# Optimization experiments

Measured on AMD Instinct MI355X. Metric: run time of the kernel, lower is better.

Reference implementation:

```python
import jax, jax.numpy as jnp
import numpy as np

B, T, E = 8, 2048, 512   # batch, tokens, embedding_dim
K, C = 8192, 8           # num_embeddings, codebook_dim
LN_EPS = 1e-5


def _layer_norm(x, g, b):
    mu = jnp.mean(x, axis=-1, keepdims=True)
    var = jnp.var(x, axis=-1, keepdims=True)
    return (x - mu) * jax.lax.rsqrt(var + LN_EPS) * g + b


def setup_inputs() -> dict:
    key = jax.random.key(0)
    ks = jax.random.split(key, 8)
    s_e = 1.0 / np.sqrt(E)
    s_c = 1.0 / np.sqrt(C)
    return {
        "features": jax.random.normal(ks[0], (B, T, E), dtype=jnp.float32),
        # project_in: Linear(E,E) -> ReLU -> Linear(E,C)
        "W1_in": jax.random.uniform(ks[1], (E, E), jnp.float32, -s_e, s_e),
        "b1_in": jnp.zeros((E,), jnp.float32),
        "W2_in": jax.random.uniform(ks[2], (E, C), jnp.float32, -s_e, s_e),
        "b2_in": jnp.zeros((C,), jnp.float32),
        "ln_in_g": jnp.ones((C,), jnp.float32),
        "ln_in_b": jnp.zeros((C,), jnp.float32),
        # codebook
        "emb": jax.random.normal(ks[3], (K, C), dtype=jnp.float32),
        # project_out: Linear(C,E) -> ReLU -> Linear(E,E)
        "W1_out": jax.random.uniform(ks[4], (C, E), jnp.float32, -s_c, s_c),
        "b1_out": jnp.zeros((E,), jnp.float32),
        "W2_out": jax.random.uniform(ks[5], (E, E), jnp.float32, -s_e, s_e),
        "b2_out": jnp.zeros((E,), jnp.float32),
        "ln_out_g": jnp.ones((E,), jnp.float32),
        "ln_out_b": jnp.zeros((E,), jnp.float32),
    }


def reference(features, W1_in, b1_in, W2_in, b2_in, ln_in_g, ln_in_b, emb,
              W1_out, b1_out, W2_out, b2_out, ln_out_g, ln_out_b):
    # project_in + norm_in
    h = jax.nn.relu(jnp.einsum('bte,ef->btf', features, W1_in) + b1_in)
    z = jnp.einsum('bte,ec->btc', h, W2_in) + b2_in          # (B,T,C)
    z = _layer_norm(z, ln_in_g, ln_in_b)
    zf = z.reshape(-1, C)                                     # (N,C)
    d = (jnp.sum(zf * zf, axis=1, keepdims=True)
         - 2.0 * zf @ emb.T
         + jnp.sum(emb * emb, axis=1)[None, :])               # (N,K)
    idx = jnp.argmin(d, axis=1)                               # (N,)
    encodings = jax.nn.one_hot(idx, K, dtype=zf.dtype)        # (N,K)
    quantized = emb[idx]                                      # gather == one_hot @ emb
    # project_out + norm_out
    q = jax.nn.relu(quantized @ W1_out + b1_out)
    q = q @ W2_out + b2_out
    q = _layer_norm(q, ln_out_g, ln_out_b)
    q = q.reshape(B, T, E)
    return q, idx[:, None], encodings
```

## Files before the change

kernel.cpp:

```cpp
#include <hip/hip_runtime.h>
#include <cstdint>
#include <cstddef>

#define N_TOK 16384
#define E_DIM 512
#define C_DIM 8
#define K_CODES 8192
#define LN_EPS 1e-5f

typedef __attribute__((ext_vector_type(8))) short short8;
typedef __attribute__((ext_vector_type(4))) float f32x4;

__device__ __forceinline__ unsigned short bf16_rn(float x) {
  unsigned u = __float_as_uint(x);
  unsigned r = u + 0x7FFFu + ((u >> 16) & 1u);
  return (unsigned short)(r >> 16);
}
__device__ __forceinline__ float bf16_f(unsigned short h) {
  return __uint_as_float(((unsigned)h) << 16);
}

__device__ __forceinline__ void gload16(const void* g, void* l) {
  __builtin_amdgcn_global_load_lds(
      (const __attribute__((address_space(1))) void*)g,
      (__attribute__((address_space(3))) void*)l, 16, 0, 0);
}

__device__ __forceinline__ void pack_a_body(const float* __restrict__ A,
    unsigned short* __restrict__ hi, unsigned short* __restrict__ lo, int t) {
  int l = t & 63;
  int kt = (t >> 6) & 15;
  int mf = t >> 10;
  const float* src = A + (size_t)(mf * 16 + (l & 15)) * 512 + kt * 32 + (l >> 4) * 8;
  float4 x0 = *(const float4*)src;
  float4 x1 = *(const float4*)(src + 4);
  float xs[8] = {x0.x, x0.y, x0.z, x0.w, x1.x, x1.y, x1.z, x1.w};
  unsigned hw[4], lw[4];
#pragma unroll
  for (int p = 0; p < 4; ++p) {
    float a = xs[2 * p], b = xs[2 * p + 1];
    unsigned short ha = bf16_rn(a), hb = bf16_rn(b);
    unsigned short la = bf16_rn(a - bf16_f(ha)), lb = bf16_rn(b - bf16_f(hb));
    hw[p] = (unsigned)ha | ((unsigned)hb << 16);
    lw[p] = (unsigned)la | ((unsigned)lb << 16);
  }
  uint4 hv; hv.x = hw[0]; hv.y = hw[1]; hv.z = hw[2]; hv.w = hw[3];
  uint4 lv; lv.x = lw[0]; lv.y = lw[1]; lv.z = lw[2]; lv.w = lw[3];
  ((uint4*)hi)[t] = hv;
  ((uint4*)lo)[t] = lv;
}

__device__ __forceinline__ void pack_b_body(const float* __restrict__ B,
    unsigned short* __restrict__ hi, unsigned short* __restrict__ lo, int t) {
  int l = t & 63;
  int kt = (t >> 6) & 15;
  int nf = t >> 10;
  int col = nf * 16 + (l & 15);
  int krow = kt * 32 + (l >> 4) * 8;
  unsigned hw[4], lw[4];
#pragma unroll
  for (int p = 0; p < 4; ++p) {
    float a = B[(size_t)(krow + 2 * p) * 512 + col];
    float b = B[(size_t)(krow + 2 * p + 1) * 512 + col];
    unsigned short ha = bf16_rn(a), hb = bf16_rn(b);
    unsigned short la = bf16_rn(a - bf16_f(ha)), lb = bf16_rn(b - bf16_f(hb));
    hw[p] = (unsigned)ha | ((unsigned)hb << 16);
    lw[p] = (unsigned)la | ((unsigned)lb << 16);
  }
  uint4 hv; hv.x = hw[0]; hv.y = hw[1]; hv.z = hw[2]; hv.w = hw[3];
  uint4 lv; lv.x = lw[0]; lv.y = lw[1]; lv.z = lw[2]; lv.w = lw[3];
  ((uint4*)hi)[t] = hv;
  ((uint4*)lo)[t] = lv;
}

__global__ __launch_bounds__(256) void prep(const float* __restrict__ features,
    const float* __restrict__ W1_in, const float* __restrict__ W2_out,
    const float* __restrict__ emb,
    unsigned short* __restrict__ A1h, unsigned short* __restrict__ A1l,
    unsigned short* __restrict__ B1h, unsigned short* __restrict__ B1l,
    unsigned short* __restrict__ B2h, unsigned short* __restrict__ B2l,
    float* __restrict__ ne) {
  int bid = blockIdx.x;
  int tid = threadIdx.x;
  if (bid < 4096) {
    pack_a_body(features, A1h, A1l, bid * 256 + tid);
  } else if (bid < 4224) {
    pack_b_body(W1_in, B1h, B1l, (bid - 4096) * 256 + tid);
  } else if (bid < 4352) {
    pack_b_body(W2_out, B2h, B2l, (bid - 4224) * 256 + tid);
  } else {
    int k = (bid - 4352) * 256 + tid;
    const float* e = emb + (size_t)k * C_DIM;
    float s = 0.f;
#pragma unroll
    for (int c = 0; c < C_DIM; ++c) s = fmaf(e[c], e[c], s);
    ne[k] = s;
  }
}

template<bool RELU>
__global__ __launch_bounds__(256) void gemm_mfma(const unsigned short* __restrict__ Ah,
    const unsigned short* __restrict__ Al, const unsigned short* __restrict__ Bh,
    const unsigned short* __restrict__ Bl, const float* __restrict__ bias,
    float* __restrict__ C) {
  __shared__ char smem[65536];
  const int tid = threadIdx.x;
  const int l = tid & 63;
  const int w = tid >> 6;
  const int wm = w >> 1, wn = w & 1;
  const int mblk = blockIdx.y, nblk = blockIdx.x;

  const char* gAh = (const char*)Ah + (((size_t)(mblk * 8 + 2 * w) * 16) * 64 + l) * 16;
  const char* gAl = (const char*)Al + (((size_t)(mblk * 8 + 2 * w) * 16) * 64 + l) * 16;
  const char* gBh = (const char*)Bh + (((size_t)(nblk * 8 + 2 * w) * 16) * 64 + l) * 16;
  const char* gBl = (const char*)Bl + (((size_t)(nblk * 8 + 2 * w) * 16) * 64 + l) * 16;

  f32x4 acc[4][4];
#pragma unroll
  for (int i = 0; i < 4; ++i)
#pragma unroll
    for (int j = 0; j < 4; ++j) acc[i][j] = (f32x4){0.f, 0.f, 0.f, 0.f};

  auto stage = [&](int buf, int kt) {
    char* base = smem + buf * 32768;
    const size_t ko = (size_t)kt * 1024;
    char* dA0 = base + (2 * w) * 1024;
    char* dA1 = base + 8192 + (2 * w) * 1024;
    char* dB0 = base + 16384 + (2 * w) * 1024;
    char* dB1 = base + 24576 + (2 * w) * 1024;
    gload16(gAh + ko,         dA0);
    gload16(gAh + ko + 16384, dA0 + 1024);
    gload16(gAl + ko,         dA1);
    gload16(gAl + ko + 16384, dA1 + 1024);
    gload16(gBh + ko,         dB0);
    gload16(gBh + ko + 16384, dB0 + 1024);
    gload16(gBl + ko,         dB1);
    gload16(gBl + ko + 16384, dB1 + 1024);
  };

  auto compute = [&](int buf) {
    const char* base = smem + buf * 32768;
    const short8* sAh = (const short8*)(base);
    const short8* sAl = (const short8*)(base + 8192);
    const short8* sBh = (const short8*)(base + 16384);
    const short8* sBl = (const short8*)(base + 24576);
    short8 a_h[4], a_l[4], b_h[4], b_l[4];
#pragma unroll
    for (int i = 0; i < 4; ++i) {
      a_h[i] = sAh[(wm * 4 + i) * 64 + l];
      a_l[i] = sAl[(wm * 4 + i) * 64 + l];
    }
#pragma unroll
    for (int j = 0; j < 4; ++j) {
      b_h[j] = sBh[(wn * 4 + j) * 64 + l];
      b_l[j] = sBl[(wn * 4 + j) * 64 + l];
    }
#pragma unroll
    for (int i = 0; i < 4; ++i)
#pragma unroll
      for (int j = 0; j < 4; ++j) {
        acc[i][j] = __builtin_amdgcn_mfma_f32_16x16x32_bf16(a_h[i], b_h[j], acc[i][j], 0, 0, 0);
        acc[i][j] = __builtin_amdgcn_mfma_f32_16x16x32_bf16(a_h[i], b_l[j], acc[i][j], 0, 0, 0);
        acc[i][j] = __builtin_amdgcn_mfma_f32_16x16x32_bf16(a_l[i], b_h[j], acc[i][j], 0, 0, 0);
      }
  };

  stage(0, 0);
  __syncthreads();
  int cur = 0;
#pragma unroll 1
  for (int kt = 1; kt < 16; ++kt) {
    stage(cur ^ 1, kt);
    compute(cur);
    __syncthreads();
    cur ^= 1;
  }
  compute(cur);

  const int colb = nblk * 128 + wn * 64 + (l & 15);
  const int rowb = mblk * 128 + wm * 64 + ((l >> 4) << 2);
#pragma unroll
  for (int j = 0; j < 4; ++j) {
    float bv = bias[colb + j * 16];
#pragma unroll
    for (int i = 0; i < 4; ++i) {
#pragma unroll
      for (int r = 0; r < 4; ++r) {
        float v = acc[i][j][r] + bv;
        if (RELU) v = fmaxf(v, 0.f);
        C[(size_t)(rowb + i * 16 + r) * 512 + colb + j * 16] = v;
      }
    }
  }
}

__global__ __launch_bounds__(256) void zln_kernel(const float* __restrict__ h,
    const float* __restrict__ W2, const float* __restrict__ b2,
    const float* __restrict__ g, const float* __restrict__ b,
    float* __restrict__ z) {
  int token = blockIdx.x * 4 + (threadIdx.x >> 6);
  int lane = threadIdx.x & 63;
  const float* hr = h + (size_t)token * E_DIM;
  float acc[C_DIM];
#pragma unroll
  for (int c = 0; c < C_DIM; ++c) acc[c] = 0.f;
  for (int e = lane; e < E_DIM; e += 64) {
    float hv = hr[e];
    const float* w = W2 + e * C_DIM;
#pragma unroll
    for (int c = 0; c < C_DIM; ++c) acc[c] = fmaf(hv, w[c], acc[c]);
  }
#pragma unroll
  for (int c = 0; c < C_DIM; ++c) {
#pragma unroll
    for (int off = 32; off > 0; off >>= 1) acc[c] += __shfl_down(acc[c], off);
  }
  if (lane == 0) {
    float v[C_DIM]; float mu = 0.f;
#pragma unroll
    for (int c = 0; c < C_DIM; ++c) { v[c] = acc[c] + b2[c]; mu += v[c]; }
    mu *= 0.125f;
    float var = 0.f;
#pragma unroll
    for (int c = 0; c < C_DIM; ++c) { float d = v[c] - mu; var += d * d; }
    var *= 0.125f;
    float inv = 1.0f / sqrtf(var + LN_EPS);
#pragma unroll
    for (int c = 0; c < C_DIM; ++c)
      z[(size_t)token * C_DIM + c] = ((v[c] - mu) * inv) * g[c] + b[c];
  }
}

__global__ __launch_bounds__(256) void vq_partial(const float* __restrict__ z,
    const float* __restrict__ emb, const float* __restrict__ ne,
    float* __restrict__ pbest, int* __restrict__ pidx) {
  int chunk = blockIdx.x & 7;
  int token = (blockIdx.x >> 3) * 256 + threadIdx.x;
  float zv[C_DIM];
#pragma unroll
  for (int c = 0; c < C_DIM; ++c) zv[c] = z[(size_t)token * C_DIM + c];
  float s = 0.f;
#pragma unroll
  for (int c = 0; c < C_DIM; ++c) s = fmaf(zv[c], zv[c], s);
  float best = 3.402823466e38f; int bi = 0;
  int j0 = chunk * 1024;
  for (int j = j0; j < j0 + 1024; ++j) {
    const float* e = emb + (size_t)j * C_DIM;
    float p = 0.f;
#pragma unroll
    for (int c = 0; c < C_DIM; ++c) p = fmaf(zv[c], e[c], p);
    float d = fmaf(-2.f, p, s) + ne[j];
    if (d < best) { best = d; bi = j; }
  }
  pbest[chunk * N_TOK + token] = best;
  pidx[chunk * N_TOK + token] = bi;
}

__global__ void vq_combine(const float* __restrict__ pbest, const int* __restrict__ pidx,
    int* __restrict__ idx_i, float* __restrict__ idxf) {
  int n = blockIdx.x * 256 + threadIdx.x;
  float best = pbest[n]; int bi = pidx[n];
#pragma unroll
  for (int c = 1; c < 8; ++c) {
    float bb = pbest[c * N_TOK + n]; int i2 = pidx[c * N_TOK + n];
    if (bb < best) { best = bb; bi = i2; }
  }
  idx_i[n] = bi;
  idxf[n] = (float)bi;
}

__global__ __launch_bounds__(256) void proj_out1_pack(const float* __restrict__ emb,
    const float* __restrict__ W1, const float* __restrict__ b1,
    unsigned short* __restrict__ hi, unsigned short* __restrict__ lo) {
  int mf = blockIdx.x;
  int l = threadIdx.x & 63;
  int kt4 = threadIdx.x >> 6;
  int k0 = mf * 16 + (l & 15);
  float ev[C_DIM];
#pragma unroll
  for (int c = 0; c < C_DIM; ++c) ev[c] = emb[(size_t)k0 * C_DIM + c];
#pragma unroll
  for (int it = 0; it < 4; ++it) {
    int kt = it * 4 + kt4;
    int e0 = kt * 32 + (l >> 4) * 8;
    float o[8];
    float4 bv0 = *(const float4*)(b1 + e0);
    float4 bv1 = *(const float4*)(b1 + e0 + 4);
    o[0] = bv0.x; o[1] = bv0.y; o[2] = bv0.z; o[3] = bv0.w;
    o[4] = bv1.x; o[5] = bv1.y; o[6] = bv1.z; o[7] = bv1.w;
#pragma unroll
    for (int c = 0; c < C_DIM; ++c) {
      float4 w0 = *(const float4*)(W1 + (size_t)c * E_DIM + e0);
      float4 w1 = *(const float4*)(W1 + (size_t)c * E_DIM + e0 + 4);
      o[0] = fmaf(ev[c], w0.x, o[0]); o[1] = fmaf(ev[c], w0.y, o[1]);
      o[2] = fmaf(ev[c], w0.z, o[2]); o[3] = fmaf(ev[c], w0.w, o[3]);
      o[4] = fmaf(ev[c], w1.x, o[4]); o[5] = fmaf(ev[c], w1.y, o[5]);
      o[6] = fmaf(ev[c], w1.z, o[6]); o[7] = fmaf(ev[c], w1.w, o[7]);
    }
    unsigned hw[4], lw[4];
#pragma unroll
    for (int p = 0; p < 4; ++p) {
      float a = fmaxf(o[2 * p], 0.f), b = fmaxf(o[2 * p + 1], 0.f);
      unsigned short ha = bf16_rn(a), hb = bf16_rn(b);
      unsigned short la = bf16_rn(a - bf16_f(ha)), lb = bf16_rn(b - bf16_f(hb));
      hw[p] = (unsigned)ha | ((unsigned)hb << 16);
      lw[p] = (unsigned)la | ((unsigned)lb << 16);
    }
    size_t t = ((size_t)mf * 16 + kt) * 64 + l;
    uint4 hv; hv.x = hw[0]; hv.y = hw[1]; hv.z = hw[2]; hv.w = hw[3];
    uint4 lv; lv.x = lw[0]; lv.y = lw[1]; lv.z = lw[2]; lv.w = lw[3];
    ((uint4*)hi)[t] = hv;
    ((uint4*)lo)[t] = lv;
  }
}

__global__ __launch_bounds__(256) void ln512(float* __restrict__ g,
    const float* __restrict__ gw, const float* __restrict__ bw) {
  int row = blockIdx.x; int tid = threadIdx.x;
  float* r = g + (size_t)row * E_DIM;
  float v0 = r[tid], v1 = r[tid + 256];
  __shared__ float red[8];
  int lane = tid & 63, wid = tid >> 6;
  float sum = v0 + v1;
#pragma unroll
  for (int off = 32; off > 0; off >>= 1) sum += __shfl_xor(sum, off);
  if (lane == 0) red[wid] = sum;
  __syncthreads();
  float mu = (red[0] + red[1] + red[2] + red[3]) * (1.0f / 512.0f);
  float d0 = v0 - mu, d1 = v1 - mu;
  float sq = d0 * d0 + d1 * d1;
#pragma unroll
  for (int off = 32; off > 0; off >>= 1) sq += __shfl_xor(sq, off);
  if (lane == 0) red[4 + wid] = sq;
  __syncthreads();
  float var = (red[4] + red[5] + red[6] + red[7]) * (1.0f / 512.0f);
  float inv = 1.0f / sqrtf(var + LN_EPS);
  r[tid]       = (d0 * inv) * gw[tid] + bw[tid];
  r[tid + 256] = (d1 * inv) * gw[tid + 256] + bw[tid + 256];
}

__global__ __launch_bounds__(128) void out_gather(const float* __restrict__ oc,
    const int* __restrict__ idx_i, float* __restrict__ q) {
  int n = blockIdx.x;
  int k = idx_i[n];
  int e = threadIdx.x * 4;
  *(float4*)(q + (size_t)n * E_DIM + e) = *(const float4*)(oc + (size_t)k * E_DIM + e);
}

__global__ void scatter_ones(const float* __restrict__ idxf, float* __restrict__ enc) {
  int n = blockIdx.x * 256 + threadIdx.x;
  int k = (int)idxf[n];
  enc[(size_t)n * K_CODES + k] = 1.0f;
}

extern "C" void kernel_launch(void* const* d_in, const int* in_sizes, int n_in,
                              void* d_out, int out_size, void* d_ws, size_t ws_size,
                              hipStream_t stream) {
  const float* features = (const float*)d_in[0];
  const float* W1_in  = (const float*)d_in[1];
  const float* b1_in  = (const float*)d_in[2];
  const float* W2_in  = (const float*)d_in[3];
  const float* b2_in  = (const float*)d_in[4];
  const float* ln_in_g = (const float*)d_in[5];
  const float* ln_in_b = (const float*)d_in[6];
  const float* emb    = (const float*)d_in[7];
  const float* W1_out = (const float*)d_in[8];
  const float* b1_out = (const float*)d_in[9];
  const float* W2_out = (const float*)d_in[10];
  const float* b2_out = (const float*)d_in[11];
  const float* ln_out_g = (const float*)d_in[12];
  const float* ln_out_b = (const float*)d_in[13];

  float* q    = (float*)d_out;
  float* idxf = q + (size_t)N_TOK * E_DIM;
  float* enc  = idxf + N_TOK;

  float* h     = enc;
  float* g     = enc + 12582912;
  float* z     = enc + 16777216;
  float* ne    = enc + 16908288;
  float* pbest = enc + 16916480;
  int*   idx_i = (int*)(enc + 17047552);
  int*   pidx  = (int*)(enc + 17063936);
  unsigned short* A1h = (unsigned short*)(enc + 17195008);
  unsigned short* A1l = (unsigned short*)(enc + 21389312);
  unsigned short* A2h = (unsigned short*)(enc + 25583616);
  unsigned short* A2l = (unsigned short*)(enc + 27680768);
  unsigned short* B1h = (unsigned short*)(enc + 29777920);
  unsigned short* B1l = (unsigned short*)(enc + 29908992);
  unsigned short* B2h = (unsigned short*)(enc + 30040064);
  unsigned short* B2l = (unsigned short*)(enc + 30171136);

  prep<<<4384, 256, 0, stream>>>(features, W1_in, W2_out, emb,
                                 A1h, A1l, B1h, B1l, B2h, B2l, ne);

  dim3 g1(4, N_TOK / 128);
  gemm_mfma<true><<<g1, 256, 0, stream>>>(A1h, A1l, B1h, B1l, b1_in, h);

  zln_kernel<<<N_TOK / 4, 256, 0, stream>>>(h, W2_in, b2_in, ln_in_g, ln_in_b, z);

  vq_partial<<<(N_TOK / 256) * 8, 256, 0, stream>>>(z, emb, ne, pbest, pidx);
  vq_combine<<<N_TOK / 256, 256, 0, stream>>>(pbest, pidx, idx_i, idxf);

  proj_out1_pack<<<K_CODES / 16, 256, 0, stream>>>(emb, W1_out, b1_out, A2h, A2l);
  dim3 g2(4, K_CODES / 128);
  gemm_mfma<false><<<g2, 256, 0, stream>>>(A2h, A2l, B2h, B2l, b2_out, g);

  ln512<<<K_CODES, 256, 0, stream>>>(g, ln_out_g, ln_out_b);

  out_gather<<<N_TOK, 128, 0, stream>>>(g, idx_i, q);

  hipMemsetAsync(enc, 0, (size_t)N_TOK * K_CODES * sizeof(float), stream);
  scatter_ones<<<N_TOK / 256, 256, 0, stream>>>(idxf, enc);
}
```

Baseline: 788.3 us.

## Fuse launches: fold codebook projection into prep, merge gather+LN and memset+scatter

Moves the per-code first output-projection pack into the prep kernel, fuses the output LayerNorm into the gather so LN runs per token rather than per code, and replaces memset plus scatter with a single kernel that zeroes each one-hot row and writes its 1. It also reorders the MFMA loops so hi/lo products issue as three separate passes. The aim is fewer kernel launches and one less pass over the codebook output, at the cost of LN work on 16384 gathered rows instead of 8192 codes.

```diff
diff --git a/kernel.cpp b/kernel.cpp
--- a/kernel.cpp
+++ b/kernel.cpp
@@ -76,9 +76,11 @@
 __global__ __launch_bounds__(256) void prep(const float* __restrict__ features,
     const float* __restrict__ W1_in, const float* __restrict__ W2_out,
     const float* __restrict__ emb,
+    const float* __restrict__ W1_out, const float* __restrict__ b1_out,
     unsigned short* __restrict__ A1h, unsigned short* __restrict__ A1l,
     unsigned short* __restrict__ B1h, unsigned short* __restrict__ B1l,
     unsigned short* __restrict__ B2h, unsigned short* __restrict__ B2l,
+    unsigned short* __restrict__ A2h, unsigned short* __restrict__ A2l,
     float* __restrict__ ne) {
   int bid = blockIdx.x;
   int tid = threadIdx.x;
@@ -88,13 +90,54 @@
     pack_b_body(W1_in, B1h, B1l, (bid - 4096) * 256 + tid);
   } else if (bid < 4352) {
     pack_b_body(W2_out, B2h, B2l, (bid - 4224) * 256 + tid);
-  } else {
+  } else if (bid < 4384) {
     int k = (bid - 4352) * 256 + tid;
     const float* e = emb + (size_t)k * C_DIM;
     float s = 0.f;
 #pragma unroll
     for (int c = 0; c < C_DIM; ++c) s = fmaf(e[c], e[c], s);
     ne[k] = s;
+  } else {
+    int mf = bid - 4384;
+    int l = tid & 63;
+    int kt4 = tid >> 6;
+    int k0 = mf * 16 + (l & 15);
+    float ev[C_DIM];
+#pragma unroll
+    for (int c = 0; c < C_DIM; ++c) ev[c] = emb[(size_t)k0 * C_DIM + c];
+#pragma unroll
+    for (int it = 0; it < 4; ++it) {
+      int kt = it * 4 + kt4;
+      int e0 = kt * 32 + (l >> 4) * 8;
+      float o[8];
+      float4 bv0 = *(const float4*)(b1_out + e0);
+      float4 bv1 = *(const float4*)(b1_out + e0 + 4);
+      o[0] = bv0.x; o[1] = bv0.y; o[2] = bv0.z; o[3] = bv0.w;
+      o[4] = bv1.x; o[5] = bv1.y; o[6] = bv1.z; o[7] = bv1.w;
+#pragma unroll
+      for (int c = 0; c < C_DIM; ++c) {
+        float4 w0 = *(const float4*)(W1_out + (size_t)c * E_DIM + e0);
+        float4 w1 = *(const float4*)(W1_out + (size_t)c * E_DIM + e0 + 4);
+        o[0] = fmaf(ev[c], w0.x, o[0]); o[1] = fmaf(ev[c], w0.y, o[1]);
+        o[2] = fmaf(ev[c], w0.z, o[2]); o[3] = fmaf(ev[c], w0.w, o[3]);
+        o[4] = fmaf(ev[c], w1.x, o[4]); o[5] = fmaf(ev[c], w1.y, o[5]);
+        o[6] = fmaf(ev[c], w1.z, o[6]); o[7] = fmaf(ev[c], w1.w, o[7]);
+      }
+      unsigned hw[4], lw[4];
+#pragma unroll
+      for (int p = 0; p < 4; ++p) {
+        float a = fmaxf(o[2 * p], 0.f), b = fmaxf(o[2 * p + 1], 0.f);
+        unsigned short ha = bf16_rn(a), hb = bf16_rn(b);
+        unsigned short la = bf16_rn(a - bf16_f(ha)), lb = bf16_rn(b - bf16_f(hb));
+        hw[p] = (unsigned)ha | ((unsigned)hb << 16);
+        lw[p] = (unsigned)la | ((unsigned)lb << 16);
+      }
+      size_t t = ((size_t)mf * 16 + kt) * 64 + l;
+      uint4 hv; hv.x = hw[0]; hv.y = hw[1]; hv.z = hw[2]; hv.w = hw[3];
+      uint4 lv; lv.x = lw[0]; lv.y = lw[1]; lv.z = lw[2]; lv.w = lw[3];
+      ((uint4*)A2h)[t] = hv;
+      ((uint4*)A2l)[t] = lv;
+    }
   }
 }
 
@@ -158,11 +201,18 @@
 #pragma unroll
     for (int i = 0; i < 4; ++i)
 #pragma unroll
-      for (int j = 0; j < 4; ++j) {
+      for (int j = 0; j < 4; ++j)
         acc[i][j] = __builtin_amdgcn_mfma_f32_16x16x32_bf16(a_h[i], b_h[j], acc[i][j], 0, 0, 0);
+#pragma unroll
+    for (int i = 0; i < 4; ++i)
+#pragma unroll
+      for (int j = 0; j < 4; ++j)
         acc[i][j] = __builtin_amdgcn_mfma_f32_16x16x32_bf16(a_h[i], b_l[j], acc[i][j], 0, 0, 0);
+#pragma unroll
+    for (int i = 0; i < 4; ++i)
+#pragma unroll
+      for (int j = 0; j < 4; ++j)
         acc[i][j] = __builtin_amdgcn_mfma_f32_16x16x32_bf16(a_l[i], b_h[j], acc[i][j], 0, 0, 0);
-      }
   };
 
   stage(0, 0);
@@ -269,88 +319,53 @@
   idxf[n] = (float)bi;
 }
 
-__global__ __launch_bounds__(256) void proj_out1_pack(const float* __restrict__ emb,
-    const float* __restrict__ W1, const float* __restrict__ b1,
-    unsigned short* __restrict__ hi, unsigned short* __restrict__ lo) {
-  int mf = blockIdx.x;
-  int l = threadIdx.x & 63;
-  int kt4 = threadIdx.x >> 6;
-  int k0 = mf * 16 + (l & 15);
-  float ev[C_DIM];
-#pragma unroll
-  for (int c = 0; c < C_DIM; ++c) ev[c] = emb[(size_t)k0 * C_DIM + c];
-#pragma unroll
-  for (int it = 0; it < 4; ++it) {
-    int kt = it * 4 + kt4;
-    int e0 = kt * 32 + (l >> 4) * 8;
-    float o[8];
-    float4 bv0 = *(const float4*)(b1 + e0);
-    float4 bv1 = *(const float4*)(b1 + e0 + 4);
-    o[0] = bv0.x; o[1] = bv0.y; o[2] = bv0.z; o[3] = bv0.w;
-    o[4] = bv1.x; o[5] = bv1.y; o[6] = bv1.z; o[7] = bv1.w;
-#pragma unroll
-    for (int c = 0; c < C_DIM; ++c) {
-      float4 w0 = *(const float4*)(W1 + (size_t)c * E_DIM + e0);
-      float4 w1 = *(const float4*)(W1 + (size_t)c * E_DIM + e0 + 4);
-      o[0] = fmaf(ev[c], w0.x, o[0]); o[1] = fmaf(ev[c], w0.y, o[1]);
-      o[2] = fmaf(ev[c], w0.z, o[2]); o[3] = fmaf(ev[c], w0.w, o[3]);
-      o[4] = fmaf(ev[c], w1.x, o[4]); o[5] = fmaf(ev[c], w1.y, o[5]);
-      o[6] = fmaf(ev[c], w1.z, o[6]); o[7] = fmaf(ev[c], w1.w, o[7]);
-    }
-    unsigned hw[4], lw[4];
-#pragma unroll
-    for (int p = 0; p < 4; ++p) {
-      float a = fmaxf(o[2 * p], 0.f), b = fmaxf(o[2 * p + 1], 0.f);
-      unsigned short ha = bf16_rn(a), hb = bf16_rn(b);
-      unsigned short la = bf16_rn(a - bf16_f(ha)), lb = bf16_rn(b - bf16_f(hb));
-      hw[p] = (unsigned)ha | ((unsigned)hb << 16);
-      lw[p] = (unsigned)la | ((unsigned)lb << 16);
-    }
-    size_t t = ((size_t)mf * 16 + kt) * 64 + l;
-    uint4 hv; hv.x = hw[0]; hv.y = hw[1]; hv.z = hw[2]; hv.w = hw[3];
-    uint4 lv; lv.x = lw[0]; lv.y = lw[1]; lv.z = lw[2]; lv.w = lw[3];
-    ((uint4*)hi)[t] = hv;
-    ((uint4*)lo)[t] = lv;
-  }
-}
-
-__global__ __launch_bounds__(256) void ln512(float* __restrict__ g,
-    const float* __restrict__ gw, const float* __restrict__ bw) {
-  int row = blockIdx.x; int tid = threadIdx.x;
-  float* r = g + (size_t)row * E_DIM;
-  float v0 = r[tid], v1 = r[tid + 256];
-  __shared__ float red[8];
+__global__ __launch_bounds__(128) void gather_ln(const float* __restrict__ oc,
+    const int* __restrict__ idx_i, const float* __restrict__ gw,
+    const float* __restrict__ bw, float* __restrict__ q) {
+  int n = blockIdx.x;
+  int tid = threadIdx.x;
+  int k = idx_i[n];
+  const float* r = oc + (size_t)k * E_DIM;
+  float4 v = ((const float4*)r)[tid];
+  __shared__ float red[4];
   int lane = tid & 63, wid = tid >> 6;
-  float sum = v0 + v1;
+  float sum = v.x + v.y + v.z + v.w;
 #pragma unroll
   for (int off = 32; off > 0; off >>= 1) sum += __shfl_xor(sum, off);
   if (lane == 0) red[wid] = sum;
   __syncthreads();
-  float mu = (red[0] + red[1] + red[2] + red[3]) * (1.0f / 512.0f);
-  float d0 = v0 - mu, d1 = v1 - mu;
-  float sq = d0 * d0 + d1 * d1;
+  float mu = (red[0] + red[1]) * (1.0f / 512.0f);
+  float4 d;
+  d.x = v.x - mu; d.y = v.y - mu; d.z = v.z - mu; d.w = v.w - mu;
+  float sq = d.x * d.x + d.y * d.y + d.z * d.z + d.w * d.w;
 #pragma unroll
   for (int off = 32; off > 0; off >>= 1) sq += __shfl_xor(sq, off);
-  if (lane == 0) red[4 + wid] = sq;
+  if (lane == 0) red[2 + wid] = sq;
   __syncthreads();
-  float var = (red[4] + red[5] + red[6] + red[7]) * (1.0f / 512.0f);
+  float var = (red[2] + red[3]) * (1.0f / 512.0f);
   float inv = 1.0f / sqrtf(var + LN_EPS);
-  r[tid]       = (d0 * inv) * gw[tid] + bw[tid];
-  r[tid + 256] = (d1 * inv) * gw[tid + 256] + bw[tid + 256];
-}
-
-__global__ __launch_bounds__(128) void out_gather(const float* __restrict__ oc,
-    const int* __restrict__ idx_i, float* __restrict__ q) {
+  float4 gg = ((const float4*)gw)[tid];
+  float4 bb = ((const float4*)bw)[tid];
+  float4 o;
+  o.x = d.x * inv * gg.x + bb.x;
+  o.y = d.y * inv * gg.y + bb.y;
+  o.z = d.z * inv * gg.z + bb.z;
+  o.w = d.w * inv * gg.w + bb.w;
+  ((float4*)(q + (size_t)n * E_DIM))[tid] = o;
+}
+
+__global__ __launch_bounds__(256) void zero_scatter(const float* __restrict__ idxf,
+    float* __restrict__ enc) {
   int n = blockIdx.x;
-  int k = idx_i[n];
-  int e = threadIdx.x * 4;
-  *(float4*)(q + (size_t)n * E_DIM + e) = *(const float4*)(oc + (size_t)k * E_DIM + e);
-}
-
-__global__ void scatter_ones(const float* __restrict__ idxf, float* __restrict__ enc) {
-  int n = blockIdx.x * 256 + threadIdx.x;
+  int tid = threadIdx.x;
   int k = (int)idxf[n];
-  enc[(size_t)n * K_CODES + k] = 1.0f;
+  float* row = enc + (size_t)n * K_CODES;
+  float4 zv = {0.f, 0.f, 0.f, 0.f};
+  int base = tid * 32;
+#pragma unroll
+  for (int u = 0; u < 8; ++u)
+    ((float4*)(row + base + u * 4))[0] = zv;
+  if ((k >> 5) == tid) row[k] = 1.0f;
 }
 
 extern "C" void kernel_launch(void* const* d_in, const int* in_sizes, int n_in,
@@ -391,8 +406,8 @@
   unsigned short* B2h = (unsigned short*)(enc + 30040064);
   unsigned short* B2l = (unsigned short*)(enc + 30171136);
 
-  prep<<<4384, 256, 0, stream>>>(features, W1_in, W2_out, emb,
-                                 A1h, A1l, B1h, B1l, B2h, B2l, ne);
+  prep<<<4896, 256, 0, stream>>>(features, W1_in, W2_out, emb, W1_out, b1_out,
+                                 A1h, A1l, B1h, B1l, B2h, B2l, A2h, A2l, ne);
 
   dim3 g1(4, N_TOK / 128);
   gemm_mfma<true><<<g1, 256, 0, stream>>>(A1h, A1l, B1h, B1l, b1_in, h);
@@ -402,14 +417,10 @@
   vq_partial<<<(N_TOK / 256) * 8, 256, 0, stream>>>(z, emb, ne, pbest, pidx);
   vq_combine<<<N_TOK / 256, 256, 0, stream>>>(pbest, pidx, idx_i, idxf);
 
-  proj_out1_pack<<<K_CODES / 16, 256, 0, stream>>>(emb, W1_out, b1_out, A2h, A2l);
   dim3 g2(4, K_CODES / 128);
   gemm_mfma<false><<<g2, 256, 0, stream>>>(A2h, A2l, B2h, B2l, b2_out, g);
 
-  ln512<<<K_CODES, 256, 0, stream>>>(g, ln_out_g, ln_out_b);
-
-  out_gather<<<N_TOK, 128, 0, stream>>>(g, idx_i, q);
-
-  hipMemsetAsync(enc, 0, (size_t)N_TOK * K_CODES * sizeof(float), stream);
-  scatter_ones<<<N_TOK / 256, 256, 0, stream>>>(idxf, enc);
-}
+  gather_ln<<<N_TOK, 128, 0, stream>>>(g, idx_i, ln_out_g, ln_out_b, q);
+
+  zero_scatter<<<N_TOK, 256, 0, stream>>>(idxf, enc);
+}
```

Result: slower. 856.5 us (+8.6%).
